# Optimization experiments

Hardware: AMD Instinct MI355X
Metric: run time of the kernel (lower is better)

The kernel has to match this reference:

```python
import jax, jax.numpy as jnp
import numpy as np

D_MODEL, D_INNER, D_STATE, D_CONV, DT_RANK = 4, 8, 16, 4, 1


def _build_perms(N, H, W):
    # center-out 2D spatial order
    yy, xx = np.meshgrid(np.arange(H), np.arange(W), indexing='ij')
    cy, cx = H // 2, W // 2
    d2 = (yy - cy) ** 2 + (xx - cx) ** 2
    sp = np.argsort(d2.reshape(-1), kind='stable')          # (H*W,)
    HW = H * W
    # scanA: for each frame t, full center-out spatial sweep
    scanA = (np.arange(N)[:, None] * HW + sp[None, :]).reshape(-1)
    # scanB: for each spatial pos (in center-out order), zig-zag over frames
    fwd = np.arange(N)
    bwd = fwd[::-1]
    tids = np.where((np.arange(HW) % 2 == 0)[:, None], fwd[None, :], bwd[None, :])  # (HW, N)
    scanB = (tids * HW + sp[:, None]).reshape(-1)
    perms = np.stack([scanA, scanB, scanA[::-1], scanB[::-1]], axis=0)  # (4, L)
    return jnp.asarray(perms)


def _dwconv1d(x_bcl, w, b, pad, groups):
    # x: (B, C, L), w: (C, 1, K) depthwise
    y = jax.lax.conv_general_dilated(x_bcl, w, (1,), [pad],
                                     feature_group_count=groups,
                                     dimension_numbers=('NCH', 'OIH', 'NCH'))
    return y + b[None, :, None]


def _forward(x, dwconv_w, dwconv_b, in_proj_w, conv1d_w, conv1d_b,
             x_proj_w, dt_proj_w, dt_proj_b, A_log, Dp, out_proj_w, ln_g, ln_b):
    B, N, H, W = x.shape
    L = N * H * W
    perms = _build_perms(N, H, W)                 # (4, L) int, static
    xf = x.reshape(B, L)
    seqs = xf[:, perms]                            # (B, 4, L) gather along 4 scans
    seqs = _dwconv1d(seqs, dwconv_w, dwconv_b, (1, 1), 4)
    u = jax.nn.silu(seqs.transpose(0, 2, 1))       # (B, L, 4)
    # ---- Mamba(d_model=4) ----
    xz = jnp.einsum('bld,ed->ble', u, in_proj_w)   # (B, L, 2*d_inner)
    xm, z = xz[..., :D_INNER], xz[..., D_INNER:]
    xc = _dwconv1d(xm.transpose(0, 2, 1), conv1d_w, conv1d_b, (D_CONV - 1, 0), D_INNER)
    xm = jax.nn.silu(xc.transpose(0, 2, 1))        # (B, L, 8) causal conv + SiLU
    x_dbl = jnp.einsum('bld,ed->ble', xm, x_proj_w)  # (B, L, dt_rank+2*d_state)
    dt = x_dbl[..., :DT_RANK]
    Bm = x_dbl[..., DT_RANK:DT_RANK + D_STATE]     # (B, L, 16)
    Cm = x_dbl[..., DT_RANK + D_STATE:]            # (B, L, 16)
    dt = jax.nn.softplus(jnp.einsum('blr,dr->bld', dt, dt_proj_w) + dt_proj_b)  # (B, L, 8)
    A = -jnp.exp(A_log)                            # (8, 16)
    dA = jnp.exp(dt[..., None] * A)                # (B, L, 8, 16)
    dBx = dt[..., None] * Bm[:, :, None, :] * xm[..., None]  # (B, L, 8, 16)

    def step(h, inp):
        dA_t, dBx_t, C_t = inp
        h = dA_t * h + dBx_t                       # (B, 8, 16)
        return h, jnp.einsum('bds,bs->bd', h, C_t)

    h0 = jnp.zeros((B, D_INNER, D_STATE), x.dtype)
    _, ys = jax.lax.scan(step, h0, (dA.transpose(1, 0, 2, 3),
                                    dBx.transpose(1, 0, 2, 3),
                                    Cm.transpose(1, 0, 2)))
    y = ys.transpose(1, 0, 2) + xm * Dp            # (B, L, 8)
    y = y * jax.nn.silu(z)
    out = jnp.einsum('bld,ed->ble', y, out_proj_w)  # (B, L, 4)
    # ---- LayerNorm(4) ----
    mu = out.mean(-1, keepdims=True)
    var = ((out - mu) ** 2).mean(-1, keepdims=True)
    out = (out - mu) * jax.lax.rsqrt(var + 1e-5) * ln_g + ln_b
    # rec[:, inv[i]] = out[:, :, i]  <=>  rec_i = out[:, perms[i], i]
    rec = jnp.take_along_axis(out, perms.T[None], axis=1)  # (B, L, 4)
    return rec.mean(-1).reshape(B, N, H, W)


def setup_inputs() -> dict:
    key = jax.random.key(0)
    ks = jax.random.split(key, 12)
    s = 0.1
    x = jax.random.normal(ks[0], (4, 6, 128, 128), jnp.float32)
    return {
        'x': x,
        'dwconv_w': jax.random.normal(ks[1], (4, 1, 3), jnp.float32) * s,
        'dwconv_b': jnp.zeros((4,), jnp.float32),
        'in_proj_w': jax.random.normal(ks[2], (2 * D_INNER, D_MODEL), jnp.float32) * s,
        'conv1d_w': jax.random.normal(ks[3], (D_INNER, 1, D_CONV), jnp.float32) * s,
        'conv1d_b': jnp.zeros((D_INNER,), jnp.float32),
        'x_proj_w': jax.random.normal(ks[4], (DT_RANK + 2 * D_STATE, D_INNER), jnp.float32) * s,
        'dt_proj_w': jax.random.normal(ks[5], (D_INNER, DT_RANK), jnp.float32) * s,
        'dt_proj_b': jnp.full((D_INNER,), -2.0, jnp.float32),
        'A_log': jnp.log(jnp.tile(jnp.arange(1, D_STATE + 1, dtype=jnp.float32), (D_INNER, 1))),
        'Dp': jnp.ones((D_INNER,), jnp.float32),
        'out_proj_w': jax.random.normal(ks[6], (D_MODEL, D_INNER), jnp.float32) * s,
        'ln_g': jnp.ones((4,), jnp.float32),
        'ln_b': jnp.zeros((4,), jnp.float32),
    }


def reference(x, dwconv_w, dwconv_b, in_proj_w, conv1d_w, conv1d_b,
              x_proj_w, dt_proj_w, dt_proj_b, A_log, Dp, out_proj_w, ln_g, ln_b):
    return _forward(x, dwconv_w, dwconv_b, in_proj_w, conv1d_w, conv1d_b,
                    x_proj_w, dt_proj_w, dt_proj_b, A_log, Dp, out_proj_w, ln_g, ln_b)
```

## Files before the change

### kernel.cpp

```cpp
#include <hip/hip_runtime.h>
#include <math.h>

#define HWSZ  16384
#define LTOT  98304
#define NB    4
#define TCH   96
#define NCH   1024
#define SD    100
#define NBL   (NB * LTOT)

__device__ __forceinline__ float siluf(float x){
  return x * __builtin_amdgcn_rcpf(1.f + __expf(-x));
}
__device__ __forceinline__ float softplusf(float x){
  return fmaxf(x, 0.f) + __logf(1.f + __expf(-fabsf(x)));
}

__device__ __forceinline__ float red16(float x){
  int v;
  v = __float_as_int(x);
  x += __int_as_float(__builtin_amdgcn_update_dpp(0, v, 0xB1, 0xF, 0xF, true));
  v = __float_as_int(x);
  x += __int_as_float(__builtin_amdgcn_update_dpp(0, v, 0x4E, 0xF, 0xF, true));
  v = __float_as_int(x);
  x += __int_as_float(__builtin_amdgcn_update_dpp(0, v, 0x141, 0xF, 0xF, true));
  v = __float_as_int(x);
  x += __int_as_float(__builtin_amdgcn_update_dpp(0, v, 0x140, 0xF, 0xF, true));
  return x;
}

__device__ __forceinline__ int isqrt_floor(int v){
  int r = __float2int_rn(sqrtf((float)v));
  if (r * r > v) --r;
  else if ((r + 1) * (r + 1) <= v) ++r;
  return r;
}

__device__ __forceinline__ int rho0(int i, const int* __restrict__ sp){
  int n = i >> 14; int r = i & (HWSZ - 1);
  return (n << 14) + sp[r];
}
__device__ __forceinline__ int rho1(int i, const int* __restrict__ sp){
  unsigned ui = (unsigned)i;
  unsigned r = ui / 6u; unsigned n = ui - r * 6u;
  unsigned t = (r & 1u) ? (5u - n) : n;
  return (int)((t << 14) + (unsigned)sp[r]);
}

__global__ __launch_bounds__(128) void k_rank(int* __restrict__ sp){
  const int j = blockIdx.x * 128 + threadIdx.x;
  const int y = j >> 7, x = j & 127;
  const int dy = y - 64, dx = x - 64;
  const int v = dy*dy + dx*dx;
  int cnt = 0;
  for (int yy = 0; yy < 128; ++yy){
    int dyy = yy - 64;
    int w = v - dyy*dyy;
    if (w > 0){
      int m = isqrt_floor(w - 1);
      int lo = m < 64 ? m : 64;
      int hi = m < 63 ? m : 63;
      cnt += lo + hi + 1;
    }
  }
  {
    const int r = isqrt_floor(v);
    int yp0 = 64 - r; if (yp0 < 0) yp0 = 0;
    int yp1 = 64 + r + 1; if (yp1 > y) yp1 = y;
    for (int yp = yp0; yp < yp1; ++yp){
      int dyp = yp - 64;
      int tt = v - dyp*dyp;
      int rr = isqrt_floor(tt);
      if (rr * rr == tt){
        cnt += (rr <= 64) ? 1 : 0;
        cnt += (rr >= 1 && rr <= 63) ? 1 : 0;
      }
    }
    if (x > 64) cnt += 1;
  }
  sp[cnt] = j;
}

__global__ __launch_bounds__(128, 4)
void k_scan(const float* __restrict__ X,
            const float* __restrict__ dww, const float* __restrict__ dwb,
            const float* __restrict__ ipw,
            const float* __restrict__ c1w, const float* __restrict__ c1b,
            const float* __restrict__ xpw,
            const float* __restrict__ dtpw, const float* __restrict__ dtpb,
            const float* __restrict__ Alog,
            const int* __restrict__ sp,
            float* __restrict__ chA, float* __restrict__ chB,
            float* __restrict__ y0g, float4* __restrict__ ug4)
{
  const int c = blockIdx.x, b = blockIdx.y;
  const int c0 = c * TCH;
  const int tid = threadIdx.x;
  const float* Xb = X + (size_t)b * LTOT;

  __shared__ __align__(16) float s_pre[(TCH + 3) * 9];
  __shared__ __align__(16) float s_dt[8 * SD];
  __shared__ __align__(16) float s_dxm[8 * SD];
  __shared__ __align__(16) float s_Bv[16 * SD];
  __shared__ __align__(16) float s_Cv[16 * SD];

  if (tid < TCH + 3){
    const int m = tid;
    const int i = c0 - 3 + m;
    if (i < 0){
      #pragma unroll
      for (int d = 0; d < 8; ++d) s_pre[m*9 + d] = 0.f;
    } else {
      const int i2 = LTOT - 1 - i;
      const bool okm = (i > 0), okp = (i < LTOT - 1);
      int q[12];
      q[0]  = okm ? rho0(i - 1, sp) : 0;
      q[1]  =       rho0(i,     sp);
      q[2]  = okp ? rho0(i + 1, sp) : 0;
      q[3]  = okm ? rho1(i - 1, sp) : 0;
      q[4]  =       rho1(i,     sp);
      q[5]  = okp ? rho1(i + 1, sp) : 0;
      q[6]  = okm ? rho0(i2 + 1, sp) : 0;
      q[7]  =       rho0(i2,     sp);
      q[8]  = okp ? rho0(i2 - 1, sp) : 0;
      q[9]  = okm ? rho1(i2 + 1, sp) : 0;
      q[10] =       rho1(i2,     sp);
      q[11] = okp ? rho1(i2 - 1, sp) : 0;
      float xv[12];
      #pragma unroll
      for (int t = 0; t < 12; ++t) xv[t] = Xb[q[t]];
      if (!okm){ xv[0] = 0.f; xv[3] = 0.f; xv[6] = 0.f; xv[9]  = 0.f; }
      if (!okp){ xv[2] = 0.f; xv[5] = 0.f; xv[8] = 0.f; xv[11] = 0.f; }
      float u[4];
      #pragma unroll
      for (int k = 0; k < 4; ++k){
        float acc = dwb[k];
        acc = fmaf(dww[k*3+0], xv[k*3+0], acc);
        acc = fmaf(dww[k*3+1], xv[k*3+1], acc);
        acc = fmaf(dww[k*3+2], xv[k*3+2], acc);
        u[k] = siluf(acc);
      }
      ug4[(size_t)b * LTOT + i] = make_float4(u[0], u[1], u[2], u[3]);
      #pragma unroll
      for (int d = 0; d < 8; ++d){
        float acc =      ipw[d*4+0] * u[0];
        acc = fmaf(ipw[d*4+1], u[1], acc);
        acc = fmaf(ipw[d*4+2], u[2], acc);
        acc = fmaf(ipw[d*4+3], u[3], acc);
        s_pre[m*9 + d] = acc;
      }
    }
  }
  __syncthreads();

  if (tid < TCH){
    const int t = tid;
    float xm[8];
    #pragma unroll
    for (int d = 0; d < 8; ++d){
      float acc = c1b[d];
      #pragma unroll
      for (int tau = 0; tau < 4; ++tau)
        acc = fmaf(c1w[d*4+tau], s_pre[(t+tau)*9 + d], acc);
      xm[d] = siluf(acc);
    }
    float dtr = xpw[0] * xm[0];
    #pragma unroll
    for (int d = 1; d < 8; ++d) dtr = fmaf(xpw[d], xm[d], dtr);
    #pragma unroll
    for (int s = 0; s < 16; ++s){
      float acc = xpw[(1+s)*8] * xm[0];
      #pragma unroll
      for (int d = 1; d < 8; ++d) acc = fmaf(xpw[(1+s)*8+d], xm[d], acc);
      s_Bv[s*SD + t] = acc;
      float acc2 = xpw[(17+s)*8] * xm[0];
      #pragma unroll
      for (int d = 1; d < 8; ++d) acc2 = fmaf(xpw[(17+s)*8+d], xm[d], acc2);
      s_Cv[s*SD + t] = acc2;
    }
    #pragma unroll
    for (int d = 0; d < 8; ++d){
      float dtv = softplusf(fmaf(dtpw[d], dtr, dtpb[d]));
      s_dt[d*SD + t]  = dtv;
      s_dxm[d*SD + t] = dtv * xm[d];
    }
  }
  __syncthreads();

  {
    const int d = tid >> 4, s = tid & 15;
    const float Ads = -__expf(Alog[tid]);
    float h = 0.f, sdt = 0.f;
    const float* pdt = s_dt + d*SD;
    const float* pdx = s_dxm + d*SD;
    const float* pB  = s_Bv + s*SD;
    const float* pC  = s_Cv + s*SD;
    float* yb = y0g + ((size_t)b * NCH + c) * 768 + d * 96;
    for (int t0 = 0; t0 < TCH; t0 += 4){
      const float4 dt4 = *reinterpret_cast<const float4*>(pdt + t0);
      const float4 dx4 = *reinterpret_cast<const float4*>(pdx + t0);
      const float4 B4  = *reinterpret_cast<const float4*>(pB + t0);
      const float4 C4  = *reinterpret_cast<const float4*>(pC + t0);
      sdt += dt4.x + dt4.y + dt4.z + dt4.w;
      float y0, y1, y2, y3;
      { float dA = __expf(dt4.x*Ads); h = fmaf(dA, h, dx4.x*B4.x); y0 = h*C4.x; }
      { float dA = __expf(dt4.y*Ads); h = fmaf(dA, h, dx4.y*B4.y); y1 = h*C4.y; }
      { float dA = __expf(dt4.z*Ads); h = fmaf(dA, h, dx4.z*B4.z); y2 = h*C4.z; }
      { float dA = __expf(dt4.w*Ads); h = fmaf(dA, h, dx4.w*B4.w); y3 = h*C4.w; }
      y0 = red16(y0); y1 = red16(y1); y2 = red16(y2); y3 = red16(y3);
      if (s == 0)
        *reinterpret_cast<float4*>(yb + t0) = make_float4(y0, y1, y2, y3);
    }
    const size_t base = ((size_t)b * NCH + c) * 128 + tid;
    chA[base] = __expf(Ads * sdt);
    chB[base] = h;
  }
}

__global__ __launch_bounds__(128) void k_comb(const float* __restrict__ chA,
                                              const float* __restrict__ chB,
                                              float* __restrict__ hin){
  const int wave = (blockIdx.x << 1) | (threadIdx.x >> 6);
  const int lane = threadIdx.x & 63;
  const int b   = wave >> 7;
  const int idx = wave & 127;
  const size_t basebi = (size_t)b * NCH * 128 + idx;
  float carry = 0.f;
  float a = chA[basebi + (size_t)lane * 128];
  float h = chB[basebi + (size_t)lane * 128];
  for (int seg = 0; seg < NCH / 64; ++seg){
    float aN = 1.f, hN = 0.f;
    if (seg + 1 < NCH / 64){
      const size_t off = basebi + (size_t)((seg + 1) * 64 + lane) * 128;
      aN = chA[off]; hN = chB[off];
    }
    #pragma unroll
    for (int o = 1; o < 64; o <<= 1){
      float aj = __shfl_up(a, o, 64);
      float hj = __shfl_up(h, o, 64);
      if (lane >= o){ h = fmaf(a, hj, h); a *= aj; }
    }
    float ae = __shfl_up(a, 1, 64);
    float he = __shfl_up(h, 1, 64);
    if (lane == 0){ ae = 1.f; he = 0.f; }
    hin[basebi + (size_t)(seg * 64 + lane) * 128] = fmaf(ae, carry, he);
    float aL = __shfl(a, 63, 64);
    float hL = __shfl(h, 63, 64);
    carry = fmaf(aL, carry, hL);
    a = aN; h = hN;
  }
}

__global__ __launch_bounds__(128, 4)
void k_corr(const float4* __restrict__ ug4,
            const float* __restrict__ ipw,
            const float* __restrict__ c1w, const float* __restrict__ c1b,
            const float* __restrict__ xpw,
            const float* __restrict__ dtpw, const float* __restrict__ dtpb,
            const float* __restrict__ Alog, const float* __restrict__ Dp,
            const float* __restrict__ opw,
            const float* __restrict__ lng, const float* __restrict__ lnb,
            const float* __restrict__ hin,
            const float* __restrict__ y0g,
            float* __restrict__ outbuf)
{
  const int c = blockIdx.x, b = blockIdx.y;
  const int c0 = c * TCH;
  const int tid = threadIdx.x;
  const size_t cb = (size_t)b * NCH + c;

  __shared__ __align__(16) float s_pre[(TCH + 3) * 9];
  __shared__ __align__(16) float s_sg[8 * 104];
  __shared__ __align__(16) float s_xm[8 * 96];
  __shared__ __align__(16) float s_Ct[96 * 20];
  __shared__ __align__(16) float s_zs[8 * 96];
  __shared__ __align__(16) float s_hA[256];
  float* s_yf = s_pre;

  s_hA[tid]       = hin[cb * 128 + tid];
  s_hA[128 + tid] = -__expf(Alog[tid]);

  if (tid < TCH + 3){
    const int m = tid;
    const int i = c0 - 3 + m;
    if (i < 0){
      #pragma unroll
      for (int d = 0; d < 8; ++d) s_pre[m*9 + d] = 0.f;
    } else {
      const float4 u4 = ug4[(size_t)b * LTOT + i];
      const float u[4] = {u4.x, u4.y, u4.z, u4.w};
      #pragma unroll
      for (int d = 0; d < 8; ++d){
        float acc =      ipw[d*4+0] * u[0];
        acc = fmaf(ipw[d*4+1], u[1], acc);
        acc = fmaf(ipw[d*4+2], u[2], acc);
        acc = fmaf(ipw[d*4+3], u[3], acc);
        s_pre[m*9 + d] = acc;
      }
      if (m >= 3){
        const int t0 = m - 3;
        #pragma unroll
        for (int d = 0; d < 8; ++d){
          float acc =      ipw[(8+d)*4+0] * u[0];
          acc = fmaf(ipw[(8+d)*4+1], u[1], acc);
          acc = fmaf(ipw[(8+d)*4+2], u[2], acc);
          acc = fmaf(ipw[(8+d)*4+3], u[3], acc);
          s_zs[d*96 + t0] = siluf(acc);
        }
      }
    }
  }
  __syncthreads();

  if (tid < TCH){
    const int t = tid;
    float xm[8];
    #pragma unroll
    for (int d = 0; d < 8; ++d){
      float acc = c1b[d];
      #pragma unroll
      for (int tau = 0; tau < 4; ++tau)
        acc = fmaf(c1w[d*4+tau], s_pre[(t+tau)*9 + d], acc);
      float v = siluf(acc);
      xm[d] = v;
      s_xm[d*96 + t] = v;
    }
    float dtr = xpw[0] * xm[0];
    #pragma unroll
    for (int d = 1; d < 8; ++d) dtr = fmaf(xpw[d], xm[d], dtr);
    float* pct = s_Ct + t*20;
    #pragma unroll
    for (int s = 0; s < 16; ++s){
      float acc2 = xpw[(17+s)*8] * xm[0];
      #pragma unroll
      for (int d = 1; d < 8; ++d) acc2 = fmaf(xpw[(17+s)*8+d], xm[d], acc2);
      pct[s] = acc2;
    }
    #pragma unroll
    for (int d = 0; d < 8; ++d)
      s_sg[d*104 + t] = softplusf(fmaf(dtpw[d], dtr, dtpb[d]));
  }
  __syncthreads();

  if (tid < 8){
    float* ps = s_sg + tid*104;
    float run = 0.f;
    for (int t0 = 0; t0 < TCH; t0 += 4){
      const float4 d4 = *reinterpret_cast<const float4*>(ps + t0);
      float r0 = run + d4.x, r1 = r0 + d4.y, r2 = r1 + d4.z, r3 = r2 + d4.w;
      *reinterpret_cast<float4*>(ps + t0) = make_float4(r0, r1, r2, r3);
      run = r3;
    }
  }
  __syncthreads();

  {
    const int d = tid >> 4, tsub = tid & 15;
    float w[16], A16[16];
    #pragma unroll
    for (int s = 0; s < 16; ++s){
      w[s]   = s_hA[d*16 + s];
      A16[s] = s_hA[128 + d*16 + s];
    }
    const float* py0 = y0g + cb * 768 + d * 96;
    for (int t = tsub; t < TCH; t += 16){
      const float sg = s_sg[d*104 + t];
      float acc = py0[t];
      const float* pc = s_Ct + t*20;
      #pragma unroll
      for (int s4 = 0; s4 < 16; s4 += 4){
        const float4 C4 = *reinterpret_cast<const float4*>(pc + s4);
        acc = fmaf(C4.x, __expf(A16[s4+0]*sg) * w[s4+0], acc);
        acc = fmaf(C4.y, __expf(A16[s4+1]*sg) * w[s4+1], acc);
        acc = fmaf(C4.z, __expf(A16[s4+2]*sg) * w[s4+2], acc);
        acc = fmaf(C4.w, __expf(A16[s4+3]*sg) * w[s4+3], acc);
      }
      s_yf[d*96 + t] = acc;
    }
  }
  __syncthreads();

  if (tid < TCH){
    const int t = tid;
    const int i = c0 + t;
    float y[8];
    #pragma unroll
    for (int d = 0; d < 8; ++d)
      y[d] = (s_yf[d*96 + t] + s_xm[d*96 + t] * Dp[d]) * s_zs[d*96 + t];
    float o[4];
    #pragma unroll
    for (int e = 0; e < 4; ++e){
      float acc = opw[e*8] * y[0];
      #pragma unroll
      for (int d = 1; d < 8; ++d) acc = fmaf(opw[e*8+d], y[d], acc);
      o[e] = acc;
    }
    const float mu = 0.25f * (o[0] + o[1] + o[2] + o[3]);
    const float v0 = o[0] - mu, v1 = o[1] - mu, v2 = o[2] - mu, v3 = o[3] - mu;
    const float inv = rsqrtf(0.25f * (v0*v0 + v1*v1 + v2*v2 + v3*v3) + 1e-5f);
    const size_t base = (size_t)b * LTOT + i;
    outbuf[0*NBL + base] = fmaf(v0 * inv, lng[0], lnb[0]);
    outbuf[1*NBL + base] = fmaf(v1 * inv, lng[1], lnb[1]);
    outbuf[2*NBL + base] = fmaf(v2 * inv, lng[2], lnb[2]);
    outbuf[3*NBL + base] = fmaf(v3 * inv, lng[3], lnb[3]);
  }
}

__global__ __launch_bounds__(256) void k_final(const float* __restrict__ outbuf,
                                               const int* __restrict__ sp,
                                               float* __restrict__ out){
  const int l = blockIdx.x * 256 + threadIdx.x;
  const int b = blockIdx.y;
  const int q0 = rho0(l, sp), q1 = rho1(l, sp);
  const int j  = LTOT - 1 - l;
  const int q2 = rho0(j, sp), q3 = rho1(j, sp);
  const size_t pb = (size_t)b * LTOT;
  out[pb + l] = 0.25f * (outbuf[0*NBL + pb + q0] + outbuf[1*NBL + pb + q1] +
                         outbuf[2*NBL + pb + q2] + outbuf[3*NBL + pb + q3]);
}

extern "C" void kernel_launch(void* const* d_in, const int* in_sizes, int n_in,
                              void* d_out, int out_size, void* d_ws, size_t ws_size,
                              hipStream_t stream) {
  const float* X    = (const float*)d_in[0];
  const float* dww  = (const float*)d_in[1];
  const float* dwb  = (const float*)d_in[2];
  const float* ipw  = (const float*)d_in[3];
  const float* c1w  = (const float*)d_in[4];
  const float* c1b  = (const float*)d_in[5];
  const float* xpw  = (const float*)d_in[6];
  const float* dtpw = (const float*)d_in[7];
  const float* dtpb = (const float*)d_in[8];
  const float* Alog = (const float*)d_in[9];
  const float* Dp   = (const float*)d_in[10];
  const float* opw  = (const float*)d_in[11];
  const float* lng  = (const float*)d_in[12];
  const float* lnb  = (const float*)d_in[13];
  float* out = (float*)d_out;

  int* wsI    = (int*)d_ws;
  int* sp     = wsI;
  float* chA  = (float*)(wsI + 16384);
  float* chB  = chA + 524288;
  float* hin  = chB + 524288;
  float4* ug4 = (float4*)(hin + 524288);
  float* y0g  = (float*)(ug4) + (size_t)NB * LTOT * 4;
  float* outbuf = y0g + 3145728;

  k_rank<<<128, 128, 0, stream>>>(sp);
  k_scan<<<dim3(NCH, NB), 128, 0, stream>>>(X, dww, dwb, ipw, c1w, c1b, xpw,
      dtpw, dtpb, Alog, sp, chA, chB, y0g, ug4);
  k_comb<<<256, 128, 0, stream>>>(chA, chB, hin);
  k_corr<<<dim3(NCH, NB), 128, 0, stream>>>(ug4, ipw, c1w, c1b, xpw,
      dtpw, dtpb, Alog, Dp, opw, lng, lnb, hin, y0g, outbuf);
  k_final<<<dim3(LTOT / 256, NB), 256, 0, stream>>>(outbuf, sp, out);
}
```

Before: 197.0 us.

## Materialize scan intermediates in global memory instead of recomputing in correction pass

The scan kernel now writes C projections, conv outputs, gated z values and per-chunk cumulative dt sums to global buffers. The correction kernel reads them back instead of recomputing from the stored u vectors. This removes the duplicated projection and conv work and two block barriers in the correction kernel. In exchange, global memory traffic grows substantially, to roughly 160 bytes per position.

```diff
diff --git a/kernel.cpp b/kernel.cpp
--- a/kernel.cpp
+++ b/kernel.cpp
@@ -91,12 +91,15 @@
             const float* __restrict__ Alog,
             const int* __restrict__ sp,
             float* __restrict__ chA, float* __restrict__ chB,
-            float* __restrict__ y0g, float4* __restrict__ ug4)
+            float* __restrict__ y0g,
+            float* __restrict__ Cg,  float* __restrict__ xmg,
+            float* __restrict__ zsg, float* __restrict__ sgg)
 {
   const int c = blockIdx.x, b = blockIdx.y;
   const int c0 = c * TCH;
   const int tid = threadIdx.x;
   const float* Xb = X + (size_t)b * LTOT;
+  const size_t cb = (size_t)b * NCH + c;
 
   __shared__ __align__(16) float s_pre[(TCH + 3) * 9];
   __shared__ __align__(16) float s_dt[8 * SD];
@@ -140,7 +143,6 @@
         acc = fmaf(dww[k*3+2], xv[k*3+2], acc);
         u[k] = siluf(acc);
       }
-      ug4[(size_t)b * LTOT + i] = make_float4(u[0], u[1], u[2], u[3]);
       #pragma unroll
       for (int d = 0; d < 8; ++d){
         float acc =      ipw[d*4+0] * u[0];
@@ -149,6 +151,21 @@
         acc = fmaf(ipw[d*4+3], u[3], acc);
         s_pre[m*9 + d] = acc;
       }
+      if (m >= 3){
+        const int t0 = m - 3;
+        float zs8[8];
+        #pragma unroll
+        for (int d = 0; d < 8; ++d){
+          float acc =      ipw[(8+d)*4+0] * u[0];
+          acc = fmaf(ipw[(8+d)*4+1], u[1], acc);
+          acc = fmaf(ipw[(8+d)*4+2], u[2], acc);
+          acc = fmaf(ipw[(8+d)*4+3], u[3], acc);
+          zs8[d] = siluf(acc);
+        }
+        float* pz = zsg + (cb*96 + t0)*8;
+        *reinterpret_cast<float4*>(pz)     = make_float4(zs8[0], zs8[1], zs8[2], zs8[3]);
+        *reinterpret_cast<float4*>(pz + 4) = make_float4(zs8[4], zs8[5], zs8[6], zs8[7]);
+      }
     }
   }
   __syncthreads();
@@ -164,9 +181,15 @@
         acc = fmaf(c1w[d*4+tau], s_pre[(t+tau)*9 + d], acc);
       xm[d] = siluf(acc);
     }
+    {
+      float* px = xmg + (cb*96 + t)*8;
+      *reinterpret_cast<float4*>(px)     = make_float4(xm[0], xm[1], xm[2], xm[3]);
+      *reinterpret_cast<float4*>(px + 4) = make_float4(xm[4], xm[5], xm[6], xm[7]);
+    }
     float dtr = xpw[0] * xm[0];
     #pragma unroll
     for (int d = 1; d < 8; ++d) dtr = fmaf(xpw[d], xm[d], dtr);
+    float C16[16];
     #pragma unroll
     for (int s = 0; s < 16; ++s){
       float acc = xpw[(1+s)*8] * xm[0];
@@ -177,6 +200,13 @@
       #pragma unroll
       for (int d = 1; d < 8; ++d) acc2 = fmaf(xpw[(17+s)*8+d], xm[d], acc2);
       s_Cv[s*SD + t] = acc2;
+      C16[s] = acc2;
+    }
+    {
+      float* pc = Cg + (cb*96 + t)*16;
+      #pragma unroll
+      for (int s4 = 0; s4 < 16; s4 += 4)
+        *reinterpret_cast<float4*>(pc + s4) = make_float4(C16[s4], C16[s4+1], C16[s4+2], C16[s4+3]);
     }
     #pragma unroll
     for (int d = 0; d < 8; ++d){
@@ -195,23 +225,27 @@
     const float* pdx = s_dxm + d*SD;
     const float* pB  = s_Bv + s*SD;
     const float* pC  = s_Cv + s*SD;
-    float* yb = y0g + ((size_t)b * NCH + c) * 768 + d * 96;
+    float* yb = y0g + cb * 768 + d * 96;
+    float* sb = sgg + (cb*8 + d) * 96;
     for (int t0 = 0; t0 < TCH; t0 += 4){
       const float4 dt4 = *reinterpret_cast<const float4*>(pdt + t0);
       const float4 dx4 = *reinterpret_cast<const float4*>(pdx + t0);
       const float4 B4  = *reinterpret_cast<const float4*>(pB + t0);
       const float4 C4  = *reinterpret_cast<const float4*>(pC + t0);
-      sdt += dt4.x + dt4.y + dt4.z + dt4.w;
+      float r0 = sdt + dt4.x, r1 = r0 + dt4.y, r2 = r1 + dt4.z, r3 = r2 + dt4.w;
+      sdt = r3;
       float y0, y1, y2, y3;
       { float dA = __expf(dt4.x*Ads); h = fmaf(dA, h, dx4.x*B4.x); y0 = h*C4.x; }
       { float dA = __expf(dt4.y*Ads); h = fmaf(dA, h, dx4.y*B4.y); y1 = h*C4.y; }
       { float dA = __expf(dt4.z*Ads); h = fmaf(dA, h, dx4.z*B4.z); y2 = h*C4.z; }
       { float dA = __expf(dt4.w*Ads); h = fmaf(dA, h, dx4.w*B4.w); y3 = h*C4.w; }
       y0 = red16(y0); y1 = red16(y1); y2 = red16(y2); y3 = red16(y3);
-      if (s == 0)
+      if (s == 0){
         *reinterpret_cast<float4*>(yb + t0) = make_float4(y0, y1, y2, y3);
-    }
-    const size_t base = ((size_t)b * NCH + c) * 128 + tid;
+        *reinterpret_cast<float4*>(sb + t0) = make_float4(r0, r1, r2, r3);
+      }
+    }
+    const size_t base = cb * 128 + tid;
     chA[base] = __expf(Ads * sdt);
     chB[base] = h;
   }
@@ -251,12 +285,9 @@
   }
 }
 
-__global__ __launch_bounds__(128, 4)
-void k_corr(const float4* __restrict__ ug4,
-            const float* __restrict__ ipw,
-            const float* __restrict__ c1w, const float* __restrict__ c1b,
-            const float* __restrict__ xpw,
-            const float* __restrict__ dtpw, const float* __restrict__ dtpb,
+__global__ __launch_bounds__(128)
+void k_corr(const float* __restrict__ Cg,  const float* __restrict__ sgg,
+            const float* __restrict__ xmg, const float* __restrict__ zsg,
             const float* __restrict__ Alog, const float* __restrict__ Dp,
             const float* __restrict__ opw,
             const float* __restrict__ lng, const float* __restrict__ lnb,
@@ -269,90 +300,11 @@
   const int tid = threadIdx.x;
   const size_t cb = (size_t)b * NCH + c;
 
-  __shared__ __align__(16) float s_pre[(TCH + 3) * 9];
-  __shared__ __align__(16) float s_sg[8 * 104];
-  __shared__ __align__(16) float s_xm[8 * 96];
-  __shared__ __align__(16) float s_Ct[96 * 20];
-  __shared__ __align__(16) float s_zs[8 * 96];
-  __shared__ __align__(16) float s_hA[256];
-  float* s_yf = s_pre;
+  __shared__ float s_hA[256];
+  __shared__ float s_yf[8 * 96];
 
   s_hA[tid]       = hin[cb * 128 + tid];
   s_hA[128 + tid] = -__expf(Alog[tid]);
-
-  if (tid < TCH + 3){
-    const int m = tid;
-    const int i = c0 - 3 + m;
-    if (i < 0){
-      #pragma unroll
-      for (int d = 0; d < 8; ++d) s_pre[m*9 + d] = 0.f;
-    } else {
-      const float4 u4 = ug4[(size_t)b * LTOT + i];
-      const float u[4] = {u4.x, u4.y, u4.z, u4.w};
-      #pragma unroll
-      for (int d = 0; d < 8; ++d){
-        float acc =      ipw[d*4+0] * u[0];
-        acc = fmaf(ipw[d*4+1], u[1], acc);
-        acc = fmaf(ipw[d*4+2], u[2], acc);
-        acc = fmaf(ipw[d*4+3], u[3], acc);
-        s_pre[m*9 + d] = acc;
-      }
-      if (m >= 3){
-        const int t0 = m - 3;
-        #pragma unroll
-        for (int d = 0; d < 8; ++d){
-          float acc =      ipw[(8+d)*4+0] * u[0];
-          acc = fmaf(ipw[(8+d)*4+1], u[1], acc);
-          acc = fmaf(ipw[(8+d)*4+2], u[2], acc);
-          acc = fmaf(ipw[(8+d)*4+3], u[3], acc);
-          s_zs[d*96 + t0] = siluf(acc);
-        }
-      }
-    }
-  }
-  __syncthreads();
-
-  if (tid < TCH){
-    const int t = tid;
-    float xm[8];
-    #pragma unroll
-    for (int d = 0; d < 8; ++d){
-      float acc = c1b[d];
-      #pragma unroll
-      for (int tau = 0; tau < 4; ++tau)
-        acc = fmaf(c1w[d*4+tau], s_pre[(t+tau)*9 + d], acc);
-      float v = siluf(acc);
-      xm[d] = v;
-      s_xm[d*96 + t] = v;
-    }
-    float dtr = xpw[0] * xm[0];
-    #pragma unroll
-    for (int d = 1; d < 8; ++d) dtr = fmaf(xpw[d], xm[d], dtr);
-    float* pct = s_Ct + t*20;
-    #pragma unroll
-    for (int s = 0; s < 16; ++s){
-      float acc2 = xpw[(17+s)*8] * xm[0];
-      #pragma unroll
-      for (int d = 1; d < 8; ++d) acc2 = fmaf(xpw[(17+s)*8+d], xm[d], acc2);
-      pct[s] = acc2;
-    }
-    #pragma unroll
-    for (int d = 0; d < 8; ++d)
-      s_sg[d*104 + t] = softplusf(fmaf(dtpw[d], dtr, dtpb[d]));
-  }
-  __syncthreads();
-
-  if (tid < 8){
-    float* ps = s_sg + tid*104;
-    float run = 0.f;
-    for (int t0 = 0; t0 < TCH; t0 += 4){
-      const float4 d4 = *reinterpret_cast<const float4*>(ps + t0);
-      float r0 = run + d4.x, r1 = r0 + d4.y, r2 = r1 + d4.z, r3 = r2 + d4.w;
-      *reinterpret_cast<float4*>(ps + t0) = make_float4(r0, r1, r2, r3);
-      run = r3;
-    }
-  }
-  __syncthreads();
 
   {
     const int d = tid >> 4, tsub = tid & 15;
@@ -362,11 +314,14 @@
       w[s]   = s_hA[d*16 + s];
       A16[s] = s_hA[128 + d*16 + s];
     }
+    const float* psg = sgg + (cb*8 + d) * 96;
     const float* py0 = y0g + cb * 768 + d * 96;
+    const float* pC  = Cg + cb * 96 * 16;
+    #pragma unroll
     for (int t = tsub; t < TCH; t += 16){
-      const float sg = s_sg[d*104 + t];
+      const float sg = psg[t];
       float acc = py0[t];
-      const float* pc = s_Ct + t*20;
+      const float* pc = pC + t*16;
       #pragma unroll
       for (int s4 = 0; s4 < 16; s4 += 4){
         const float4 C4 = *reinterpret_cast<const float4*>(pc + s4);
@@ -383,10 +338,18 @@
   if (tid < TCH){
     const int t = tid;
     const int i = c0 + t;
+    const float* px = xmg + (cb*96 + t)*8;
+    const float* pz = zsg + (cb*96 + t)*8;
+    const float4 xa = *reinterpret_cast<const float4*>(px);
+    const float4 xbv = *reinterpret_cast<const float4*>(px + 4);
+    const float4 za = *reinterpret_cast<const float4*>(pz);
+    const float4 zb = *reinterpret_cast<const float4*>(pz + 4);
+    const float xm8[8] = {xa.x, xa.y, xa.z, xa.w, xbv.x, xbv.y, xbv.z, xbv.w};
+    const float zs8[8] = {za.x, za.y, za.z, za.w, zb.x, zb.y, zb.z, zb.w};
     float y[8];
     #pragma unroll
     for (int d = 0; d < 8; ++d)
-      y[d] = (s_yf[d*96 + t] + s_xm[d*96 + t] * Dp[d]) * s_zs[d*96 + t];
+      y[d] = (s_yf[d*96 + t] + xm8[d] * Dp[d]) * zs8[d];
     float o[4];
     #pragma unroll
     for (int e = 0; e < 4; ++e){
@@ -443,15 +406,18 @@
   float* chA  = (float*)(wsI + 16384);
   float* chB  = chA + 524288;
   float* hin  = chB + 524288;
-  float4* ug4 = (float4*)(hin + 524288);
-  float* y0g  = (float*)(ug4) + (size_t)NB * LTOT * 4;
-  float* outbuf = y0g + 3145728;
+  float* y0g  = hin + 524288;
+  float* Cg   = y0g + 3145728;
+  float* xmg  = Cg  + 6291456;
+  float* zsg  = xmg + 3145728;
+  float* sgg  = zsg + 3145728;
+  float* outbuf = sgg + 3145728;
 
   k_rank<<<128, 128, 0, stream>>>(sp);
   k_scan<<<dim3(NCH, NB), 128, 0, stream>>>(X, dww, dwb, ipw, c1w, c1b, xpw,
-      dtpw, dtpb, Alog, sp, chA, chB, y0g, ug4);
+      dtpw, dtpb, Alog, sp, chA, chB, y0g, Cg, xmg, zsg, sgg);
   k_comb<<<256, 128, 0, stream>>>(chA, chB, hin);
-  k_corr<<<dim3(NCH, NB), 128, 0, stream>>>(ug4, ipw, c1w, c1b, xpw,
-      dtpw, dtpb, Alog, Dp, opw, lng, lnb, hin, y0g, outbuf);
+  k_corr<<<dim3(NCH, NB), 128, 0, stream>>>(Cg, sgg, xmg, zsg,
+      Alog, Dp, opw, lng, lnb, hin, y0g, outbuf);
   k_final<<<dim3(LTOT / 256, NB), 256, 0, stream>>>(outbuf, sp, out);
 }
```

Result: faster. 192.4 us (-2.3%).
